# Optimization experiments

Measured on AMD Instinct MI355X. Metric: run time of the kernel, lower is better.

Reference implementation:

```python
import jax, jax.numpy as jnp
import numpy as np

WINDOW_SIZE = 11
SIGMA = 1.5
C1 = (0.01 * 1.0) ** 2
C2 = (0.03 * 1.0) ** 2


def _gauss1d(k, sigma):
    x = np.arange(k, dtype=np.float64) - k // 2
    g = np.exp(-(x ** 2) / (2.0 * sigma ** 2)) / (np.sqrt(2.0 * np.pi) * sigma)
    return (g / g.sum()).astype(np.float32)


def _blur3d(x, g):
    # Separable 3D Gaussian blur, SAME padding. Math-equal to the full 11^3
    # kernel conv in the torch code since the 3D window is an outer product
    # of the normalized 1D Gaussian (symmetric, so conv == cross-corr).
    k = g.shape[0]
    p = k // 2
    dn = ('NCDHW', 'OIDHW', 'NCDHW')
    for axis in range(3):
        shape = [1, 1, 1, 1, 1]
        shape[2 + axis] = k
        w = jnp.asarray(g).reshape(shape)
        pad = [(0, 0), (0, 0), (0, 0)]
        pad[axis] = (p, p)
        x = jax.lax.conv_general_dilated(x, w, (1, 1, 1), pad, dimension_numbers=dn)
    return x


def setup_inputs() -> dict:
    key = jax.random.key(0)
    k1, k2 = jax.random.split(key)
    shape = (4, 1, 192, 192, 192)
    gt = jax.random.uniform(k1, shape, dtype=jnp.float32)
    pred = jax.random.uniform(k2, shape, dtype=jnp.float32)
    return {"gt": gt, "pred": pred}


def reference(gt, pred):
    g = _gauss1d(WINDOW_SIZE, SIGMA)
    mux = _blur3d(gt, g)
    muy = _blur3d(pred, g)
    mux_sq = mux * mux
    muy_sq = muy * muy
    mux_muy = mux * muy
    sigmax_sq = _blur3d(gt * gt, g) - mux_sq
    sigmay_sq = _blur3d(pred * pred, g) - muy_sq
    sigmaxy = _blur3d(gt * pred, g) - mux_muy
    ssim_map = ((2.0 * mux_muy + C1) * (2.0 * sigmaxy + C2)) / (
        (mux_sq + muy_sq + C1) * (sigmax_sq + sigmay_sq + C2))
    return jnp.mean(1.0 - ssim_map)
```

## Files before the change

### kernel.cpp

```cpp
#include <hip/hip_runtime.h>
#include <hip/hip_fp16.h>
#include <math.h>

namespace {
constexpr int S = 192;
constexpr long long S2 = (long long)S * S;
constexpr long long S3 = (long long)S * S2;
constexpr int NB = 4;
constexpr int K = 11;
constexpr int R = 5;
constexpr int HCH = 32;
constexpr int DCH = 48;
constexpr float C1f = 1e-4f;
constexpr float C2f = 9e-4f;

struct GaussW { float g[K]; };

__global__ void k_init(double* acc) { *acc = 0.0; }

__global__ void k_final(const double* __restrict__ acc, float* __restrict__ out) {
  out[0] = (float)(acc[0] / (double)(NB * S3));
}


template <int NROWS, bool GUARD>
__device__ __forceinline__ void stageA(const float* pg, const float* pp, int r0,
                                       int w, float2 (*rb)[208]) {
  float la[NROWS], lb[NROWS];
#pragma unroll
  for (int j = 0; j < NROWS; ++j) {
    int r = r0 + j;
    bool ok = !GUARD || ((unsigned)r < (unsigned)S);
    la[j] = ok ? pg[(long long)r * S + w] : 0.f;
    lb[j] = ok ? pp[(long long)r * S + w] : 0.f;
  }
#pragma unroll
  for (int j = 0; j < NROWS; ++j) rb[j][8 + w] = make_float2(la[j], lb[j]);
}

template <int NROWS, bool EMITALL>
__device__ __forceinline__ void consumeA(
    const float2 (*rb)[208], int w, const GaussW& Wt,
    float2 (&w01)[K], float2 (&w23)[K], float (&w4v)[K],
    uint2* p0123, __half* p4, long long obase, int hbase) {
#pragma unroll
  for (int j = 0; j < NROWS; ++j) {
    float2 s01 = make_float2(0.f, 0.f), s23 = make_float2(0.f, 0.f);
    float s4 = 0.f;
#pragma unroll
    for (int i = 0; i < K; ++i) {
      float2 ab = rb[j][w + 3 + i];
      float g = Wt.g[i];
      s01.x = fmaf(g, ab.x, s01.x);
      s01.y = fmaf(g, ab.y, s01.y);
      float ta = g * ab.x, tb = g * ab.y;
      s23.x = fmaf(ta, ab.x, s23.x);
      s23.y = fmaf(tb, ab.y, s23.y);
      s4 = fmaf(ta, ab.y, s4);
    }
    w01[j] = s01; w23[j] = s23; w4v[j] = s4;
    if (EMITALL || j == K - 1) {
      float2 m01 = make_float2(0.f, 0.f), m23 = make_float2(0.f, 0.f);
      float m4 = 0.f;
#pragma unroll
      for (int i = 0; i < K; ++i) {
        const int sl = (j + 1 + i) % K;
        float g = Wt.g[i];
        m01.x = fmaf(g, w01[sl].x, m01.x);
        m01.y = fmaf(g, w01[sl].y, m01.y);
        m23.x = fmaf(g, w23[sl].x, m23.x);
        m23.y = fmaf(g, w23[sl].y, m23.y);
        m4 = fmaf(g, w4v[sl], m4);
      }
      long long o = obase + (long long)(hbase + j) * S;
      __half2 h01 = __floats2half2_rn(m01.x, m01.y);
      __half2 h23 = __floats2half2_rn(m23.x, m23.y);
      uint2 v;
      v.x = __builtin_bit_cast(unsigned, h01);
      v.y = __builtin_bit_cast(unsigned, h23);
      p0123[o] = v;
      p4[o] = __float2half(m4);
    }
  }
}

__global__ __launch_bounds__(192) void k_blurWH(
    const float* __restrict__ gt, const float* __restrict__ pr,
    uint2* __restrict__ p0123, __half* __restrict__ p4,
    long long in_base, GaussW Wt) {
  __shared__ float2 rowbuf[K][208];
  const int w = threadIdx.x;
  const int dz = blockIdx.x;
  const int h0 = (int)blockIdx.y * HCH;
  const long long n = blockIdx.z;
  const float* pg = gt + in_base + (n * S + dz) * S2;
  const float* pp = pr + in_base + (n * S + dz) * S2;
  const long long obase = (n * S + dz) * S2 + w;

  if (w < 176) {
    int j = w >> 4, q = w & 15;
    rowbuf[j][(q < 8) ? q : (192 + q)] = make_float2(0.f, 0.f);
  }

  float2 w01[K], w23[K];
  float w4v[K];

  stageA<K, true>(pg, pp, h0 - R, w, rowbuf);
  __syncthreads();
  consumeA<K, false>(rowbuf, w, Wt, w01, w23, w4v, p0123, p4, obase, h0 - 10);
  __syncthreads();
  stageA<K, false>(pg, pp, h0 + 6, w, rowbuf);
  __syncthreads();
  consumeA<K, true>(rowbuf, w, Wt, w01, w23, w4v, p0123, p4, obase, h0 + 1);
  __syncthreads();
  stageA<K, false>(pg, pp, h0 + 17, w, rowbuf);
  __syncthreads();
  consumeA<K, true>(rowbuf, w, Wt, w01, w23, w4v, p0123, p4, obase, h0 + 12);
  __syncthreads();
  stageA<9, true>(pg, pp, h0 + 28, w, rowbuf);
  __syncthreads();
  consumeA<9, true>(rowbuf, w, Wt, w01, w23, w4v, p0123, p4, obase, h0 + 23);
}


template <int N, bool GUARD>
__device__ __forceinline__ void stageB(const uint2* q0123, const __half* q4,
                                       int plane0, uint2 (&sab)[K], __half (&se)[K]) {
#pragma unroll
  for (int j = 0; j < N; ++j) {
    int d = plane0 + j;
    bool ok = !GUARD || ((unsigned)d < (unsigned)S);
    long long o = (long long)d * S2;
    sab[j] = ok ? q0123[o] : make_uint2(0u, 0u);
    se[j] = ok ? q4[o] : __float2half(0.f);
  }
}

template <int NOUT>
__device__ __forceinline__ void consumeB(
    const uint2 (&sab)[K], const __half (&se)[K],
    const GaussW& Wt, float2 (&r01)[K], float2 (&r23)[K], float (&r4)[K],
    double& lsum) {
  float fsum = 0.f;
#pragma unroll
  for (int j = 0; j < NOUT; ++j) {
    const int sw = (10 + j) % K;
    r01[sw] = __half22float2(__builtin_bit_cast(__half2, sab[j].x));
    r23[sw] = __half22float2(__builtin_bit_cast(__half2, sab[j].y));
    r4[sw] = __half2float(se[j]);
    float2 m01 = make_float2(0.f, 0.f), m23 = make_float2(0.f, 0.f);
    float m4 = 0.f;
#pragma unroll
    for (int i = 0; i < K; ++i) {
      const int sl = (j + i) % K;
      float g = Wt.g[i];
      m01.x = fmaf(g, r01[sl].x, m01.x);
      m01.y = fmaf(g, r01[sl].y, m01.y);
      m23.x = fmaf(g, r23[sl].x, m23.x);
      m23.y = fmaf(g, r23[sl].y, m23.y);
      m4 = fmaf(g, r4[sl], m4);
    }
    float mux = m01.x, muy = m01.y, bxx = m23.x, byy = m23.y, bxy = m4;
    float mux2 = mux * mux, muy2 = muy * muy, muxy = mux * muy;
    float sx = bxx - mux2, sy = byy - muy2, sxy = bxy - muxy;
    float num = fmaf(2.f, muxy, C1f) * fmaf(2.f, sxy, C2f);
    float den = (mux2 + muy2 + C1f) * (sx + sy + C2f);
    fsum += 1.f - num * __builtin_amdgcn_rcpf(den);
  }
  lsum += (double)fsum;
}

__global__ __launch_bounds__(192) void k_blurD_ssim(
    const uint2* __restrict__ p0123, const __half* __restrict__ p4,
    double* __restrict__ acc, GaussW Wt) {
  const int w = threadIdx.x;
  const int h = blockIdx.x;
  const long long n = blockIdx.y;
  const int d0 = (int)blockIdx.z * DCH;
  const long long base = n * S3 + (long long)h * S + w;
  const uint2* q0123 = p0123 + base;
  const __half* q4 = p4 + base;

  float2 r01[K], r23[K];
  float r4[K];
#pragma unroll
  for (int c = 0; c < K - 1; ++c) {
    int d = d0 - R + c;
    if ((unsigned)d < (unsigned)S) {
      long long o = (long long)d * S2;
      uint2 v = q0123[o];
      r01[c] = __half22float2(__builtin_bit_cast(__half2, v.x));
      r23[c] = __half22float2(__builtin_bit_cast(__half2, v.y));
      r4[c] = __half2float(q4[o]);
    } else {
      r01[c] = make_float2(0.f, 0.f);
      r23[c] = make_float2(0.f, 0.f);
      r4[c] = 0.f;
    }
  }
  r01[K - 1] = make_float2(0.f, 0.f);
  r23[K - 1] = make_float2(0.f, 0.f);
  r4[K - 1] = 0.f;

  uint2 sab0[K], sab1[K];
  __half se0[K], se1[K];
  double lsum = 0.0;

  stageB<K, false>(q0123, q4, d0 + 5, sab0, se0);
  stageB<K, false>(q0123, q4, d0 + 16, sab1, se1);
  consumeB<K>(sab0, se0, Wt, r01, r23, r4, lsum);
  stageB<K, false>(q0123, q4, d0 + 27, sab0, se0);
  consumeB<K>(sab1, se1, Wt, r01, r23, r4, lsum);
  stageB<K, true>(q0123, q4, d0 + 38, sab1, se1);
  consumeB<K>(sab0, se0, Wt, r01, r23, r4, lsum);
  stageB<4, true>(q0123, q4, d0 + 49, sab0, se0);
  consumeB<K>(sab1, se1, Wt, r01, r23, r4, lsum);
  consumeB<4>(sab0, se0, Wt, r01, r23, r4, lsum);

  double v = lsum;
#pragma unroll
  for (int o = 32; o > 0; o >>= 1) v += __shfl_down(v, o, 64);
  __shared__ double wsum[3];
  int lane = threadIdx.x & 63, wv = threadIdx.x >> 6;
  if (lane == 0) wsum[wv] = v;
  __syncthreads();
  if (threadIdx.x == 0) atomicAdd(acc, wsum[0] + wsum[1] + wsum[2]);
}

}

extern "C" void kernel_launch(void* const* d_in, const int* in_sizes, int n_in,
                              void* d_out, int out_size, void* d_ws, size_t ws_size,
                              hipStream_t stream) {
  (void)in_sizes; (void)n_in; (void)out_size;
  const float* gt = (const float*)d_in[0];
  const float* pr = (const float*)d_in[1];
  float* out = (float*)d_out;
  double* acc = (double*)d_ws;

  GaussW W;
  {
    double gg[K], sum = 0.0;
    for (int i = 0; i < K; ++i) {
      double x = (double)(i - K / 2);
      gg[i] = exp(-(x * x) / (2.0 * 1.5 * 1.5)) / (sqrt(2.0 * M_PI) * 1.5);
      sum += gg[i];
    }
    for (int i = 0; i < K; ++i) W.g[i] = (float)(gg[i] / sum);
  }

  auto run = [&](long long base_n, int nb) {
    size_t vox = (size_t)nb * S3;
    uint2* p0123 = (uint2*)((char*)d_ws + 256);
    __half* p4 = (__half*)(p0123 + vox);
    k_blurWH<<<dim3(S, S / HCH, nb), dim3(192), 0, stream>>>(
        gt, pr, p0123, p4, base_n * S3, W);
    k_blurD_ssim<<<dim3(S, nb, S / DCH), dim3(192), 0, stream>>>(
        p0123, p4, acc, W);
  };
  auto need = [](int nb) { return (size_t)256 + (size_t)nb * S3 * 10; };

  k_init<<<dim3(1), dim3(1), 0, stream>>>(acc);
  if (ws_size >= need(4)) {
    run(0, 4);
  } else if (ws_size >= need(2)) {
    run(0, 2);
    run(2, 2);
  } else {
    for (int g = 0; g < NB; ++g) run(g, 1);
  }
  k_final<<<dim3(1), dim3(1), 0, stream>>>(acc, out);
}
```

Baseline: 429.2 us.

## Use packed fp16 math in W/H blur, double-buffer row staging, enlarge H chunk

```diff
diff --git a/kernel.cpp b/kernel.cpp
--- a/kernel.cpp
+++ b/kernel.cpp
@@ -9,7 +9,7 @@
 constexpr int NB = 4;
 constexpr int K = 11;
 constexpr int R = 5;
-constexpr int HCH = 32;
+constexpr int HCH = 48;
 constexpr int DCH = 48;
 constexpr float C1f = 1e-4f;
 constexpr float C2f = 9e-4f;
@@ -23,63 +23,62 @@
 }
 
 
-template <int NROWS, bool GUARD>
-__device__ __forceinline__ void stageA(const float* pg, const float* pp, int r0,
-                                       int w, float2 (*rb)[208]) {
-  float la[NROWS], lb[NROWS];
-#pragma unroll
-  for (int j = 0; j < NROWS; ++j) {
+template <int N, bool GUARD>
+__device__ __forceinline__ void loadA(const float* pg, const float* pp, int r0,
+                                      int w, __half2 (&lh)[K]) {
+#pragma unroll
+  for (int j = 0; j < N; ++j) {
     int r = r0 + j;
     bool ok = !GUARD || ((unsigned)r < (unsigned)S);
-    la[j] = ok ? pg[(long long)r * S + w] : 0.f;
-    lb[j] = ok ? pp[(long long)r * S + w] : 0.f;
-  }
-#pragma unroll
-  for (int j = 0; j < NROWS; ++j) rb[j][8 + w] = make_float2(la[j], lb[j]);
+    float a = ok ? pg[(long long)r * S + w] : 0.f;
+    float b = ok ? pp[(long long)r * S + w] : 0.f;
+    lh[j] = __floats2half2_rn(a, b);
+  }
+}
+
+template <int N>
+__device__ __forceinline__ void commitA(__half2 (*rb)[208], int w,
+                                        const __half2 (&lh)[K]) {
+#pragma unroll
+  for (int j = 0; j < N; ++j) rb[j][8 + w] = lh[j];
 }
 
 template <int NROWS, bool EMITALL>
 __device__ __forceinline__ void consumeA(
-    const float2 (*rb)[208], int w, const GaussW& Wt,
-    float2 (&w01)[K], float2 (&w23)[K], float (&w4v)[K],
+    const __half2 (*rb)[208], int w, const __half2 (&gh2)[K],
+    __half2 (&q01)[K], __half2 (&q23)[K], __half (&q4)[K],
     uint2* p0123, __half* p4, long long obase, int hbase) {
 #pragma unroll
   for (int j = 0; j < NROWS; ++j) {
-    float2 s01 = make_float2(0.f, 0.f), s23 = make_float2(0.f, 0.f);
-    float s4 = 0.f;
+    __half2 s01 = __floats2half2_rn(0.f, 0.f);
+    __half2 s23 = s01;
+    __half s4 = __float2half(0.f);
 #pragma unroll
     for (int i = 0; i < K; ++i) {
-      float2 ab = rb[j][w + 3 + i];
-      float g = Wt.g[i];
-      s01.x = fmaf(g, ab.x, s01.x);
-      s01.y = fmaf(g, ab.y, s01.y);
-      float ta = g * ab.x, tb = g * ab.y;
-      s23.x = fmaf(ta, ab.x, s23.x);
-      s23.y = fmaf(tb, ab.y, s23.y);
-      s4 = fmaf(ta, ab.y, s4);
-    }
-    w01[j] = s01; w23[j] = s23; w4v[j] = s4;
+      __half2 ab = rb[j][w + 3 + i];
+      s01 = __hfma2(gh2[i], ab, s01);
+      __half2 t = __hmul2(gh2[i], ab);
+      s23 = __hfma2(t, ab, s23);
+      s4 = __hfma(__low2half(t), __high2half(ab), s4);
+    }
+    q01[j] = s01; q23[j] = s23; q4[j] = s4;
     if (EMITALL || j == K - 1) {
-      float2 m01 = make_float2(0.f, 0.f), m23 = make_float2(0.f, 0.f);
-      float m4 = 0.f;
+      __half2 m01 = __floats2half2_rn(0.f, 0.f);
+      __half2 m23 = m01;
+      __half m4 = __float2half(0.f);
 #pragma unroll
       for (int i = 0; i < K; ++i) {
         const int sl = (j + 1 + i) % K;
-        float g = Wt.g[i];
-        m01.x = fmaf(g, w01[sl].x, m01.x);
-        m01.y = fmaf(g, w01[sl].y, m01.y);
-        m23.x = fmaf(g, w23[sl].x, m23.x);
-        m23.y = fmaf(g, w23[sl].y, m23.y);
-        m4 = fmaf(g, w4v[sl], m4);
+        m01 = __hfma2(gh2[i], q01[sl], m01);
+        m23 = __hfma2(gh2[i], q23[sl], m23);
+        m4 = __hfma(__low2half(gh2[i]), q4[sl], m4);
       }
       long long o = obase + (long long)(hbase + j) * S;
-      __half2 h01 = __floats2half2_rn(m01.x, m01.y);
-      __half2 h23 = __floats2half2_rn(m23.x, m23.y);
       uint2 v;
-      v.x = __builtin_bit_cast(unsigned, h01);
-      v.y = __builtin_bit_cast(unsigned, h23);
+      v.x = __builtin_bit_cast(unsigned, m01);
+      v.y = __builtin_bit_cast(unsigned, m23);
       p0123[o] = v;
-      p4[o] = __float2half(m4);
+      p4[o] = m4;
     }
   }
 }
@@ -88,7 +87,7 @@
     const float* __restrict__ gt, const float* __restrict__ pr,
     uint2* __restrict__ p0123, __half* __restrict__ p4,
     long long in_base, GaussW Wt) {
-  __shared__ float2 rowbuf[K][208];
+  __shared__ __half2 rowbuf[2][K][208];
   const int w = threadIdx.x;
   const int dz = blockIdx.x;
   const int h0 = (int)blockIdx.y * HCH;
@@ -97,29 +96,45 @@
   const float* pp = pr + in_base + (n * S + dz) * S2;
   const long long obase = (n * S + dz) * S2 + w;
 
+  __half2 gh2[K];
+#pragma unroll
+  for (int i = 0; i < K; ++i) gh2[i] = __float2half2_rn(Wt.g[i]);
+
   if (w < 176) {
     int j = w >> 4, q = w & 15;
-    rowbuf[j][(q < 8) ? q : (192 + q)] = make_float2(0.f, 0.f);
-  }
-
-  float2 w01[K], w23[K];
-  float w4v[K];
-
-  stageA<K, true>(pg, pp, h0 - R, w, rowbuf);
-  __syncthreads();
-  consumeA<K, false>(rowbuf, w, Wt, w01, w23, w4v, p0123, p4, obase, h0 - 10);
-  __syncthreads();
-  stageA<K, false>(pg, pp, h0 + 6, w, rowbuf);
-  __syncthreads();
-  consumeA<K, true>(rowbuf, w, Wt, w01, w23, w4v, p0123, p4, obase, h0 + 1);
-  __syncthreads();
-  stageA<K, false>(pg, pp, h0 + 17, w, rowbuf);
-  __syncthreads();
-  consumeA<K, true>(rowbuf, w, Wt, w01, w23, w4v, p0123, p4, obase, h0 + 12);
-  __syncthreads();
-  stageA<9, true>(pg, pp, h0 + 28, w, rowbuf);
-  __syncthreads();
-  consumeA<9, true>(rowbuf, w, Wt, w01, w23, w4v, p0123, p4, obase, h0 + 23);
+    int idx = (q < 8) ? q : (192 + q);
+    rowbuf[0][j][idx] = __floats2half2_rn(0.f, 0.f);
+    rowbuf[1][j][idx] = __floats2half2_rn(0.f, 0.f);
+  }
+
+  __half2 q01[K], q23[K];
+  __half q4[K];
+  __half2 lh[K];
+
+  loadA<K, true>(pg, pp, h0 - R, w, lh);
+  commitA<K>(rowbuf[0], w, lh);
+  __syncthreads();
+  loadA<K, false>(pg, pp, h0 + 6, w, lh);
+  consumeA<K, false>(rowbuf[0], w, gh2, q01, q23, q4, p0123, p4, obase, h0 - 10);
+  commitA<K>(rowbuf[1], w, lh);
+  __syncthreads();
+  loadA<K, false>(pg, pp, h0 + 17, w, lh);
+  consumeA<K, true>(rowbuf[1], w, gh2, q01, q23, q4, p0123, p4, obase, h0 + 1);
+  commitA<K>(rowbuf[0], w, lh);
+  __syncthreads();
+  loadA<K, false>(pg, pp, h0 + 28, w, lh);
+  consumeA<K, true>(rowbuf[0], w, gh2, q01, q23, q4, p0123, p4, obase, h0 + 12);
+  commitA<K>(rowbuf[1], w, lh);
+  __syncthreads();
+  loadA<K, true>(pg, pp, h0 + 39, w, lh);
+  consumeA<K, true>(rowbuf[1], w, gh2, q01, q23, q4, p0123, p4, obase, h0 + 23);
+  commitA<K>(rowbuf[0], w, lh);
+  __syncthreads();
+  loadA<3, true>(pg, pp, h0 + 50, w, lh);
+  consumeA<K, true>(rowbuf[0], w, gh2, q01, q23, q4, p0123, p4, obase, h0 + 34);
+  commitA<3>(rowbuf[1], w, lh);
+  __syncthreads();
+  consumeA<3, true>(rowbuf[1], w, gh2, q01, q23, q4, p0123, p4, obase, h0 + 45);
 }
 
 
```

New measurement: 508.0 us. 18.4% more time.

## Stage all halo rows at once in fp16 shared buffer, single barrier

Applied to the files above, without the earlier changes.

```diff
diff --git a/kernel.cpp b/kernel.cpp
--- a/kernel.cpp
+++ b/kernel.cpp
@@ -10,6 +10,7 @@
 constexpr int K = 11;
 constexpr int R = 5;
 constexpr int HCH = 32;
+constexpr int RW = HCH + 2 * R;
 constexpr int DCH = 48;
 constexpr float C1f = 1e-4f;
 constexpr float C2f = 9e-4f;
@@ -20,75 +21,13 @@
 
 __global__ void k_final(const double* __restrict__ acc, float* __restrict__ out) {
   out[0] = (float)(acc[0] / (double)(NB * S3));
-}
-
-
-template <int NROWS, bool GUARD>
-__device__ __forceinline__ void stageA(const float* pg, const float* pp, int r0,
-                                       int w, float2 (*rb)[208]) {
-  float la[NROWS], lb[NROWS];
-#pragma unroll
-  for (int j = 0; j < NROWS; ++j) {
-    int r = r0 + j;
-    bool ok = !GUARD || ((unsigned)r < (unsigned)S);
-    la[j] = ok ? pg[(long long)r * S + w] : 0.f;
-    lb[j] = ok ? pp[(long long)r * S + w] : 0.f;
-  }
-#pragma unroll
-  for (int j = 0; j < NROWS; ++j) rb[j][8 + w] = make_float2(la[j], lb[j]);
-}
-
-template <int NROWS, bool EMITALL>
-__device__ __forceinline__ void consumeA(
-    const float2 (*rb)[208], int w, const GaussW& Wt,
-    float2 (&w01)[K], float2 (&w23)[K], float (&w4v)[K],
-    uint2* p0123, __half* p4, long long obase, int hbase) {
-#pragma unroll
-  for (int j = 0; j < NROWS; ++j) {
-    float2 s01 = make_float2(0.f, 0.f), s23 = make_float2(0.f, 0.f);
-    float s4 = 0.f;
-#pragma unroll
-    for (int i = 0; i < K; ++i) {
-      float2 ab = rb[j][w + 3 + i];
-      float g = Wt.g[i];
-      s01.x = fmaf(g, ab.x, s01.x);
-      s01.y = fmaf(g, ab.y, s01.y);
-      float ta = g * ab.x, tb = g * ab.y;
-      s23.x = fmaf(ta, ab.x, s23.x);
-      s23.y = fmaf(tb, ab.y, s23.y);
-      s4 = fmaf(ta, ab.y, s4);
-    }
-    w01[j] = s01; w23[j] = s23; w4v[j] = s4;
-    if (EMITALL || j == K - 1) {
-      float2 m01 = make_float2(0.f, 0.f), m23 = make_float2(0.f, 0.f);
-      float m4 = 0.f;
-#pragma unroll
-      for (int i = 0; i < K; ++i) {
-        const int sl = (j + 1 + i) % K;
-        float g = Wt.g[i];
-        m01.x = fmaf(g, w01[sl].x, m01.x);
-        m01.y = fmaf(g, w01[sl].y, m01.y);
-        m23.x = fmaf(g, w23[sl].x, m23.x);
-        m23.y = fmaf(g, w23[sl].y, m23.y);
-        m4 = fmaf(g, w4v[sl], m4);
-      }
-      long long o = obase + (long long)(hbase + j) * S;
-      __half2 h01 = __floats2half2_rn(m01.x, m01.y);
-      __half2 h23 = __floats2half2_rn(m23.x, m23.y);
-      uint2 v;
-      v.x = __builtin_bit_cast(unsigned, h01);
-      v.y = __builtin_bit_cast(unsigned, h23);
-      p0123[o] = v;
-      p4[o] = __float2half(m4);
-    }
-  }
 }
 
 __global__ __launch_bounds__(192) void k_blurWH(
     const float* __restrict__ gt, const float* __restrict__ pr,
     uint2* __restrict__ p0123, __half* __restrict__ p4,
     long long in_base, GaussW Wt) {
-  __shared__ float2 rowbuf[K][208];
+  __shared__ __half2 rowbuf[RW][208];
   const int w = threadIdx.x;
   const int dz = blockIdx.x;
   const int h0 = (int)blockIdx.y * HCH;
@@ -97,29 +36,67 @@
   const float* pp = pr + in_base + (n * S + dz) * S2;
   const long long obase = (n * S + dz) * S2 + w;
 
-  if (w < 176) {
-    int j = w >> 4, q = w & 15;
-    rowbuf[j][(q < 8) ? q : (192 + q)] = make_float2(0.f, 0.f);
-  }
+#pragma unroll
+  for (int j = 0; j < RW; ++j) {
+    const int r = h0 - R + j;
+    __half2 v = __floats2half2_rn(0.f, 0.f);
+    if ((unsigned)r < (unsigned)S) {
+      v = __floats2half2_rn(pg[(long long)r * S + w], pp[(long long)r * S + w]);
+    }
+    rowbuf[j][8 + w] = v;
+  }
+#pragma unroll
+  for (int t = 0; t < 4; ++t) {
+    const int idx = t * 192 + w;
+    if (idx < RW * 16) {
+      const int row = idx >> 4, q = idx & 15;
+      rowbuf[row][(q < 8) ? q : (192 + q)] = __floats2half2_rn(0.f, 0.f);
+    }
+  }
+  __syncthreads();
 
   float2 w01[K], w23[K];
   float w4v[K];
-
-  stageA<K, true>(pg, pp, h0 - R, w, rowbuf);
-  __syncthreads();
-  consumeA<K, false>(rowbuf, w, Wt, w01, w23, w4v, p0123, p4, obase, h0 - 10);
-  __syncthreads();
-  stageA<K, false>(pg, pp, h0 + 6, w, rowbuf);
-  __syncthreads();
-  consumeA<K, true>(rowbuf, w, Wt, w01, w23, w4v, p0123, p4, obase, h0 + 1);
-  __syncthreads();
-  stageA<K, false>(pg, pp, h0 + 17, w, rowbuf);
-  __syncthreads();
-  consumeA<K, true>(rowbuf, w, Wt, w01, w23, w4v, p0123, p4, obase, h0 + 12);
-  __syncthreads();
-  stageA<9, true>(pg, pp, h0 + 28, w, rowbuf);
-  __syncthreads();
-  consumeA<9, true>(rowbuf, w, Wt, w01, w23, w4v, p0123, p4, obase, h0 + 23);
+#pragma unroll
+  for (int c = 0; c < RW; ++c) {
+    float2 s01 = make_float2(0.f, 0.f), s23 = make_float2(0.f, 0.f);
+    float s4 = 0.f;
+#pragma unroll
+    for (int i = 0; i < K; ++i) {
+      const __half2 abh = rowbuf[c][w + 3 + i];
+      const float a = __half2float(__low2half(abh));
+      const float b = __half2float(__high2half(abh));
+      const float g = Wt.g[i];
+      s01.x = fmaf(g, a, s01.x);
+      s01.y = fmaf(g, b, s01.y);
+      const float ta = g * a, tb = g * b;
+      s23.x = fmaf(ta, a, s23.x);
+      s23.y = fmaf(tb, b, s23.y);
+      s4 = fmaf(ta, b, s4);
+    }
+    const int sl0 = c % K;
+    w01[sl0] = s01; w23[sl0] = s23; w4v[sl0] = s4;
+    if (c >= K - 1) {
+      float2 m01 = make_float2(0.f, 0.f), m23 = make_float2(0.f, 0.f);
+      float m4 = 0.f;
+#pragma unroll
+      for (int i = 0; i < K; ++i) {
+        const int sl = (c + 1 + i) % K;
+        const float g = Wt.g[i];
+        m01.x = fmaf(g, w01[sl].x, m01.x);
+        m01.y = fmaf(g, w01[sl].y, m01.y);
+        m23.x = fmaf(g, w23[sl].x, m23.x);
+        m23.y = fmaf(g, w23[sl].y, m23.y);
+        m4 = fmaf(g, w4v[sl], m4);
+      }
+      const long long o = obase + (long long)(h0 + c - 2 * R) * S;
+      uint2 v;
+      v.x = __builtin_bit_cast(unsigned, __floats2half2_rn(m01.x, m01.y));
+      v.y = __builtin_bit_cast(unsigned, __floats2half2_rn(m23.x, m23.y));
+      p0123[o] = v;
+      p4[o] = __float2half(m4);
+    }
+  }
 }
 
 
```

After: 520.4 us. 1.21x slower.
